# Kernel tuning notes

Measured on AMD Instinct MI355X. Metric: run time of the kernel, lower is better.

Reference implementation:

```python
import jax, jax.numpy as jnp
import numpy as np

B, I, O, D, H = 64, 1152, 32, 8, 16
NUM_ITERS = 3


def squash(s, axis=-1, eps=1e-08):
    sq = jnp.sum(s * s, axis=axis, keepdims=True)
    return (sq / (1.0 + sq)) * s / jnp.sqrt(sq + eps)


def setup_inputs() -> dict:
    key = jax.random.key(0)
    k1, k2 = jax.random.split(key)
    u = jax.random.normal(k1, (B, I, D), dtype=jnp.float32)
    weight = jax.random.normal(k2, (I, O, D, H), dtype=jnp.float32) * 0.1
    return {"u": u, "weight": weight}


def reference(u, weight):
    # u_hat: [b, i, o, h]
    u_hat = jnp.einsum('bid,iodh->bioh', u, weight)
    logits = jnp.zeros(u_hat.shape[:3], dtype=u_hat.dtype)

    def body(logits, _):
        coupling = jax.nn.softmax(logits, axis=-1)        # [b,i,o]
        s = jnp.einsum('bio,bioh->boh', coupling, u_hat)  # [b,o,h]
        v = squash(s)                                     # [b,o,h]
        logits = logits + jnp.einsum('boh,bioh->bio', v, u_hat)
        return logits, v

    _, vs = jax.lax.scan(body, logits, None, length=NUM_ITERS)
    return vs[-1]
```

## Files before the change

### kernel.cpp

```cpp
#include <hip/hip_runtime.h>
#include <hip/hip_bf16.h>

#define BB 64
#define II 1152
#define OO 32
#define DD 8
#define HH 16
#define BOH (BB * OO * HH)
#define WTILE (OO * DD * HH)

#define IC   9
#define NIC  128
#define NBB  16
#define NBG  4
#define NJB  4
#define WS   132

__device__ __forceinline__ float row_sum16(float x)
{
    x += __int_as_float(__builtin_amdgcn_update_dpp(
            0, __float_as_int(x), 0x121, 0xF, 0xF, false));
    x += __int_as_float(__builtin_amdgcn_update_dpp(
            0, __float_as_int(x), 0x122, 0xF, 0xF, false));
    x += __int_as_float(__builtin_amdgcn_update_dpp(
            0, __float_as_int(x), 0x124, 0xF, 0xF, false));
    x += __int_as_float(__builtin_amdgcn_update_dpp(
            0, __float_as_int(x), 0x128, 0xF, 0xF, false));
    return x;
}

__device__ __forceinline__ float o_sum32(float x)
{
    float s = row_sum16(x);
    s += __int_as_float(__builtin_amdgcn_ds_swizzle(__float_as_int(s), 0x401F));
    return s;
}

template<int PASS, bool ATOMIC>
__global__ __launch_bounds__(256)
void pass_kernel(const float* __restrict__ u, const float* __restrict__ w,
                 const float* __restrict__ pv0, const float* __restrict__ pv1,
                 float* __restrict__ out)
{
    __shared__ float Wsh[2][OO * WS];

    const int tid   = threadIdx.x;
    const int o     = tid & 31;
    const int hh    = (tid >> 5) & 1;
    const int bq    = tid >> 6;
    const int bbase = blockIdx.y * NBB;
    const int i0    = blockIdx.x * IC;
    const int hofs  = hh * 8;

    float vsum[NJB][8];
    if (PASS >= 1) {
        #pragma unroll
        for (int jb = 0; jb < NJB; jb++) {
            const int b = bbase + bq * NJB + jb;
            const float* p = pv0 + ((b * OO + o) * HH + hofs);
            float4 a = *(const float4*)p;
            float4 c = *(const float4*)(p + 4);
            vsum[jb][0] = a.x; vsum[jb][1] = a.y; vsum[jb][2] = a.z; vsum[jb][3] = a.w;
            vsum[jb][4] = c.x; vsum[jb][5] = c.y; vsum[jb][6] = c.z; vsum[jb][7] = c.w;
            if (PASS == 2) {
                const float* q = pv1 + ((b * OO + o) * HH + hofs);
                float4 a2 = *(const float4*)q;
                float4 c2 = *(const float4*)(q + 4);
                vsum[jb][0] += a2.x; vsum[jb][1] += a2.y; vsum[jb][2] += a2.z; vsum[jb][3] += a2.w;
                vsum[jb][4] += c2.x; vsum[jb][5] += c2.y; vsum[jb][6] += c2.z; vsum[jb][7] += c2.w;
            }
        }
    }

    float sacc[NJB][8];
    #pragma unroll
    for (int jb = 0; jb < NJB; jb++)
        #pragma unroll
        for (int h2 = 0; h2 < 8; h2++) sacc[jb][h2] = 0.f;

    {
        const float* wg = w + (size_t)i0 * WTILE;
        #pragma unroll
        for (int j = 0; j < 4; j++) {
            const int c = tid + j * 256;
            float4 v4 = *(const float4*)(wg + c * 4);
            *(float4*)&Wsh[0][(c >> 5) * WS + (c & 31) * 4] = v4;
        }
    }
    __syncthreads();

    for (int ii = 0; ii < IC; ii++) {
        const float* wcur = Wsh[ii & 1];
        const bool pf = (ii + 1 < IC);
        float4 t0, t1, t2, t3;
        if (pf) {
            const float* wg = w + (size_t)(i0 + ii + 1) * WTILE;
            t0 = *(const float4*)(wg + (tid      ) * 4);
            t1 = *(const float4*)(wg + (tid + 256) * 4);
            t2 = *(const float4*)(wg + (tid + 512) * 4);
            t3 = *(const float4*)(wg + (tid + 768) * 4);
        }

        float us[NJB][8];
        #pragma unroll
        for (int jb = 0; jb < NJB; jb++) {
            const float* ub = u + ((size_t)(bbase + bq * NJB + jb) * II + (i0 + ii)) * DD;
            float4 a = *(const float4*)ub;
            float4 c = *(const float4*)(ub + 4);
            us[jb][0] = a.x; us[jb][1] = a.y; us[jb][2] = a.z; us[jb][3] = a.w;
            us[jb][4] = c.x; us[jb][5] = c.y; us[jb][6] = c.z; us[jb][7] = c.w;
        }

        float uh[NJB][8];
        #pragma unroll
        for (int jb = 0; jb < NJB; jb++)
            #pragma unroll
            for (int h2 = 0; h2 < 8; h2++) uh[jb][h2] = 0.f;
        #pragma unroll
        for (int d = 0; d < DD; d++) {
            const float* wp = &wcur[o * WS + d * HH + hofs];
            float4 wa = *(const float4*)wp;
            float4 wb = *(const float4*)(wp + 4);
            const float wv[8] = {wa.x, wa.y, wa.z, wa.w, wb.x, wb.y, wb.z, wb.w};
            #pragma unroll
            for (int jb = 0; jb < NJB; jb++)
                #pragma unroll
                for (int h2 = 0; h2 < 8; h2++)
                    uh[jb][h2] = fmaf(us[jb][d], wv[h2], uh[jb][h2]);
        }

        float cc[NJB];
        if (PASS == 0) {
            #pragma unroll
            for (int jb = 0; jb < NJB; jb++) cc[jb] = 1.0f / 32.0f;
        } else {
            #pragma unroll
            for (int jb = 0; jb < NJB; jb++) {
                float lg = 0.f;
                #pragma unroll
                for (int h2 = 0; h2 < 8; h2++)
                    lg = fmaf(vsum[jb][h2], uh[jb][h2], lg);
                lg += __shfl_xor(lg, 32, 64);
                const float e = __expf(lg);
                const float se = o_sum32(e);
                cc[jb] = __fdividef(e, se);
            }
        }

        #pragma unroll
        for (int jb = 0; jb < NJB; jb++)
            #pragma unroll
            for (int h2 = 0; h2 < 8; h2++)
                sacc[jb][h2] = fmaf(cc[jb], uh[jb][h2], sacc[jb][h2]);

        if (pf) {
            float* wn = Wsh[(ii + 1) & 1];
            const int c0 = tid, c1 = tid + 256, c2 = tid + 512, c3 = tid + 768;
            *(float4*)&wn[(c0 >> 5) * WS + (c0 & 31) * 4] = t0;
            *(float4*)&wn[(c1 >> 5) * WS + (c1 & 31) * 4] = t1;
            *(float4*)&wn[(c2 >> 5) * WS + (c2 & 31) * 4] = t2;
            *(float4*)&wn[(c3 >> 5) * WS + (c3 & 31) * 4] = t3;
        }
        __syncthreads();
    }

    #pragma unroll
    for (int jb = 0; jb < NJB; jb++) {
        const int b = bbase + bq * NJB + jb;
        if (ATOMIC) {
            float* p = out + ((b * OO + o) * HH + hofs);
            #pragma unroll
            for (int h2 = 0; h2 < 8; h2++) atomicAdd(p + h2, sacc[jb][h2]);
        } else {
            float* p = out + ((size_t)blockIdx.x * BB + b) * (OO * HH) + o * HH + hofs;
            *(float4*)p       = make_float4(sacc[jb][0], sacc[jb][1], sacc[jb][2], sacc[jb][3]);
            *(float4*)(p + 4) = make_float4(sacc[jb][4], sacc[jb][5], sacc[jb][6], sacc[jb][7]);
        }
    }
}

__global__ __launch_bounds__(256)
void reduce_squash_kernel(const float* __restrict__ part, float* __restrict__ v)
{
    const int t = blockIdx.x * blockDim.x + threadIdx.x;
    float acc = 0.f;
    #pragma unroll 16
    for (int ic = 0; ic < NIC; ic++)
        acc += part[(size_t)ic * BOH + t];
    const float sq = row_sum16(acc * acc);
    const float scale = (sq / (1.f + sq)) * rsqrtf(sq + 1e-8f);
    v[t] = acc * scale;
}

__global__ __launch_bounds__(256)
void squash_kernel(const float* __restrict__ s, float* __restrict__ v)
{
    const int t = blockIdx.x * blockDim.x + threadIdx.x;
    if (t >= BB * OO) return;
    const float4* sp = (const float4*)(s + t * HH);
    float4 a = sp[0], b = sp[1], c = sp[2], d = sp[3];
    float sq = a.x*a.x + a.y*a.y + a.z*a.z + a.w*a.w
             + b.x*b.x + b.y*b.y + b.z*b.z + b.w*b.w
             + c.x*c.x + c.y*c.y + c.z*c.z + c.w*c.w
             + d.x*d.x + d.y*d.y + d.z*d.z + d.w*d.w;
    const float scale = (sq / (1.f + sq)) * rsqrtf(sq + 1e-8f);
    a.x *= scale; a.y *= scale; a.z *= scale; a.w *= scale;
    b.x *= scale; b.y *= scale; b.z *= scale; b.w *= scale;
    c.x *= scale; c.y *= scale; c.z *= scale; c.w *= scale;
    d.x *= scale; d.y *= scale; d.z *= scale; d.w *= scale;
    float4* vp = (float4*)(v + t * HH);
    vp[0] = a; vp[1] = b; vp[2] = c; vp[3] = d;
}

extern "C" void kernel_launch(void* const* d_in, const int* in_sizes, int n_in,
                              void* d_out, int out_size, void* d_ws, size_t ws_size,
                              hipStream_t stream)
{
    (void)in_sizes; (void)n_in; (void)out_size;
    const float* u = (const float*)d_in[0];
    const float* w = (const float*)d_in[1];
    float* out = (float*)d_out;

    const size_t need = ((size_t)NIC * BOH + 2 * BOH) * sizeof(float);
    const dim3 grid(NIC, NBG), blk(256);

    if (ws_size >= need) {
        float* part = (float*)d_ws;
        float* v0   = part + (size_t)NIC * BOH;
        float* v1   = v0 + BOH;
        const int rblocks = BOH / 256;

        pass_kernel<0, false><<<grid, blk, 0, stream>>>(u, w, nullptr, nullptr, part);
        reduce_squash_kernel<<<rblocks, 256, 0, stream>>>(part, v0);
        pass_kernel<1, false><<<grid, blk, 0, stream>>>(u, w, v0, nullptr, part);
        reduce_squash_kernel<<<rblocks, 256, 0, stream>>>(part, v1);
        pass_kernel<2, false><<<grid, blk, 0, stream>>>(u, w, v0, v1, part);
        reduce_squash_kernel<<<rblocks, 256, 0, stream>>>(part, out);
    } else {
        float* s0 = (float*)d_ws;
        float* s1 = s0 + BOH;
        float* v0 = s1 + BOH;
        float* v1 = v0 + BOH;
        hipMemsetAsync(d_ws, 0, 2 * BOH * sizeof(float), stream);
        hipMemsetAsync(d_out, 0, BOH * sizeof(float), stream);
        const int sq_blocks = (BB * OO + 255) / 256;

        pass_kernel<0, true><<<grid, blk, 0, stream>>>(u, w, nullptr, nullptr, s0);
        squash_kernel<<<sq_blocks, 256, 0, stream>>>(s0, v0);
        pass_kernel<1, true><<<grid, blk, 0, stream>>>(u, w, v0, nullptr, s1);
        squash_kernel<<<sq_blocks, 256, 0, stream>>>(s1, v1);
        pass_kernel<2, true><<<grid, blk, 0, stream>>>(u, w, v0, v1, out);
        squash_kernel<<<sq_blocks, 256, 0, stream>>>(out, out);
    }
}
```

Measured before the change: 142.1 us.

## Convert weights to bf16 in first pass and reuse for later routing passes

The first pass now also writes a bf16 copy of the weight tensor to workspace. Passes 1 and 2 run a new kernel that reads the half-size bf16 weights, converts them to fp32 in registers, and splits the input dimension into more chunks (192 instead of 128) for more parallelism. The goal is to halve weight memory traffic in the later passes, at the cost of reduced weight precision, extra writes in pass 0, a larger workspace, and a larger partial-sum reduction.

Measured after the change: 186.8 us. 31.4% more time.

```diff
diff --git a/kernel.cpp b/kernel.cpp
--- a/kernel.cpp
+++ b/kernel.cpp
@@ -9,26 +9,34 @@
 #define BOH (BB * OO * HH)
 #define WTILE (OO * DD * HH)
 
-#define IC   9
-#define NIC  128
+#define IC0  9
+#define NIC0 128
+#define IC2  6
+#define NIC2 192
 #define NBB  16
 #define NBG  4
 #define NJB  4
 #define WS   132
+#define WSB  136
+#define TBF  4352
+
+__device__ __forceinline__ unsigned bfpack(float a, float b)
+{
+    unsigned ua = __float_as_uint(a); ua += 0x7FFFu + ((ua >> 16) & 1u);
+    unsigned ub = __float_as_uint(b); ub += 0x7FFFu + ((ub >> 16) & 1u);
+    return (ua >> 16) | (ub & 0xFFFF0000u);
+}
+__device__ __forceinline__ float bflo(unsigned x) { return __uint_as_float(x << 16); }
+__device__ __forceinline__ float bfhi(unsigned x) { return __uint_as_float(x & 0xFFFF0000u); }
 
 __device__ __forceinline__ float row_sum16(float x)
 {
-    x += __int_as_float(__builtin_amdgcn_update_dpp(
-            0, __float_as_int(x), 0x121, 0xF, 0xF, false));
-    x += __int_as_float(__builtin_amdgcn_update_dpp(
-            0, __float_as_int(x), 0x122, 0xF, 0xF, false));
-    x += __int_as_float(__builtin_amdgcn_update_dpp(
-            0, __float_as_int(x), 0x124, 0xF, 0xF, false));
-    x += __int_as_float(__builtin_amdgcn_update_dpp(
-            0, __float_as_int(x), 0x128, 0xF, 0xF, false));
+    x += __int_as_float(__builtin_amdgcn_update_dpp(0, __float_as_int(x), 0x121, 0xF, 0xF, false));
+    x += __int_as_float(__builtin_amdgcn_update_dpp(0, __float_as_int(x), 0x122, 0xF, 0xF, false));
+    x += __int_as_float(__builtin_amdgcn_update_dpp(0, __float_as_int(x), 0x124, 0xF, 0xF, false));
+    x += __int_as_float(__builtin_amdgcn_update_dpp(0, __float_as_int(x), 0x128, 0xF, 0xF, false));
     return x;
 }
-
 __device__ __forceinline__ float o_sum32(float x)
 {
     float s = row_sum16(x);
@@ -40,7 +48,7 @@
 __global__ __launch_bounds__(256)
 void pass_kernel(const float* __restrict__ u, const float* __restrict__ w,
                  const float* __restrict__ pv0, const float* __restrict__ pv1,
-                 float* __restrict__ out)
+                 float* __restrict__ out, unsigned* __restrict__ wb)
 {
     __shared__ float Wsh[2][OO * WS];
 
@@ -49,8 +57,9 @@
     const int hh    = (tid >> 5) & 1;
     const int bq    = tid >> 6;
     const int bbase = blockIdx.y * NBB;
-    const int i0    = blockIdx.x * IC;
+    const int i0    = blockIdx.x * IC0;
     const int hofs  = hh * 8;
+    const bool cvt  = (wb != nullptr) && (blockIdx.y == 0);
 
     float vsum[NJB][8];
     if (PASS >= 1) {
@@ -85,13 +94,17 @@
             const int c = tid + j * 256;
             float4 v4 = *(const float4*)(wg + c * 4);
             *(float4*)&Wsh[0][(c >> 5) * WS + (c & 31) * 4] = v4;
+            if (cvt) {
+                uint2 p2 = make_uint2(bfpack(v4.x, v4.y), bfpack(v4.z, v4.w));
+                *(uint2*)(wb + (size_t)i0 * 2048 + c * 2) = p2;
+            }
         }
     }
     __syncthreads();
 
-    for (int ii = 0; ii < IC; ii++) {
+    for (int ii = 0; ii < IC0; ii++) {
         const float* wcur = Wsh[ii & 1];
-        const bool pf = (ii + 1 < IC);
+        const bool pf = (ii + 1 < IC0);
         float4 t0, t1, t2, t3;
         if (pf) {
             const float* wg = w + (size_t)(i0 + ii + 1) * WTILE;
@@ -120,8 +133,8 @@
         for (int d = 0; d < DD; d++) {
             const float* wp = &wcur[o * WS + d * HH + hofs];
             float4 wa = *(const float4*)wp;
-            float4 wb = *(const float4*)(wp + 4);
-            const float wv[8] = {wa.x, wa.y, wa.z, wa.w, wb.x, wb.y, wb.z, wb.w};
+            float4 wc = *(const float4*)(wp + 4);
+            const float wv[8] = {wa.x, wa.y, wa.z, wa.w, wc.x, wc.y, wc.z, wc.w};
             #pragma unroll
             for (int jb = 0; jb < NJB; jb++)
                 #pragma unroll
@@ -160,6 +173,13 @@
             *(float4*)&wn[(c1 >> 5) * WS + (c1 & 31) * 4] = t1;
             *(float4*)&wn[(c2 >> 5) * WS + (c2 & 31) * 4] = t2;
             *(float4*)&wn[(c3 >> 5) * WS + (c3 & 31) * 4] = t3;
+            if (cvt) {
+                unsigned* wt = wb + (size_t)(i0 + ii + 1) * 2048;
+                *(uint2*)(wt + c0 * 2) = make_uint2(bfpack(t0.x, t0.y), bfpack(t0.z, t0.w));
+                *(uint2*)(wt + c1 * 2) = make_uint2(bfpack(t1.x, t1.y), bfpack(t1.z, t1.w));
+                *(uint2*)(wt + c2 * 2) = make_uint2(bfpack(t2.x, t2.y), bfpack(t2.z, t2.w));
+                *(uint2*)(wt + c3 * 2) = make_uint2(bfpack(t3.x, t3.y), bfpack(t3.z, t3.w));
+            }
         }
         __syncthreads();
     }
@@ -179,13 +199,152 @@
     }
 }
 
+template<int PASS>
+__global__ __launch_bounds__(256)
+void pass_bf(const float* __restrict__ u, const unsigned* __restrict__ wb,
+             const float* __restrict__ pv0, const float* __restrict__ pv1,
+             float* __restrict__ out)
+{
+    __shared__ unsigned short Wb[2][2 * TBF];
+
+    const int tid   = threadIdx.x;
+    const int o     = tid & 31;
+    const int hh    = (tid >> 5) & 1;
+    const int bq    = tid >> 6;
+    const int bbase = blockIdx.y * NBB;
+    const int i0    = blockIdx.x * IC2;
+    const int hofs  = hh * 8;
+
+    float vsum[NJB][8];
+    #pragma unroll
+    for (int jb = 0; jb < NJB; jb++) {
+        const int b = bbase + bq * NJB + jb;
+        const float* p = pv0 + ((b * OO + o) * HH + hofs);
+        float4 a = *(const float4*)p;
+        float4 c = *(const float4*)(p + 4);
+        vsum[jb][0] = a.x; vsum[jb][1] = a.y; vsum[jb][2] = a.z; vsum[jb][3] = a.w;
+        vsum[jb][4] = c.x; vsum[jb][5] = c.y; vsum[jb][6] = c.z; vsum[jb][7] = c.w;
+        if (PASS == 2) {
+            const float* q = pv1 + ((b * OO + o) * HH + hofs);
+            float4 a2 = *(const float4*)q;
+            float4 c2 = *(const float4*)(q + 4);
+            vsum[jb][0] += a2.x; vsum[jb][1] += a2.y; vsum[jb][2] += a2.z; vsum[jb][3] += a2.w;
+            vsum[jb][4] += c2.x; vsum[jb][5] += c2.y; vsum[jb][6] += c2.z; vsum[jb][7] += c2.w;
+        }
+    }
+
+    float sacc[NJB][8];
+    #pragma unroll
+    for (int jb = 0; jb < NJB; jb++)
+        #pragma unroll
+        for (int h2 = 0; h2 < 8; h2++) sacc[jb][h2] = 0.f;
+
+    {
+        const uint4* wg = (const uint4*)(wb + (size_t)i0 * 2048);
+        #pragma unroll
+        for (int j = 0; j < 4; j++) {
+            const int c  = tid + j * 256;
+            uint4 v4 = wg[c];
+            const int cc = c & 511;
+            *(uint4*)&Wb[0][(c >> 9) * TBF + (cc >> 4) * WSB + (cc & 15) * 8] = v4;
+        }
+    }
+    __syncthreads();
+
+    for (int s = 0; s < IC2 / 2; s++) {
+        const unsigned short* wbuf = Wb[s & 1];
+        const bool pf = (s + 1 < IC2 / 2);
+        uint4 t0, t1, t2, t3;
+        if (pf) {
+            const uint4* wg = (const uint4*)(wb + (size_t)(i0 + 2 * s + 2) * 2048);
+            t0 = wg[tid];
+            t1 = wg[tid + 256];
+            t2 = wg[tid + 512];
+            t3 = wg[tid + 768];
+        }
+
+        #pragma unroll
+        for (int it = 0; it < 2; it++) {
+            const int i = i0 + 2 * s + it;
+            const unsigned short* wt = &wbuf[it * TBF + o * WSB + hofs];
+
+            float us[NJB][8];
+            #pragma unroll
+            for (int jb = 0; jb < NJB; jb++) {
+                const float* ub = u + ((size_t)(bbase + bq * NJB + jb) * II + i) * DD;
+                float4 a = *(const float4*)ub;
+                float4 c = *(const float4*)(ub + 4);
+                us[jb][0] = a.x; us[jb][1] = a.y; us[jb][2] = a.z; us[jb][3] = a.w;
+                us[jb][4] = c.x; us[jb][5] = c.y; us[jb][6] = c.z; us[jb][7] = c.w;
+            }
+
+            float uh[NJB][8];
+            #pragma unroll
+            for (int jb = 0; jb < NJB; jb++)
+                #pragma unroll
+                for (int h2 = 0; h2 < 8; h2++) uh[jb][h2] = 0.f;
+            #pragma unroll
+            for (int d = 0; d < DD; d++) {
+                const uint4 wd = *(const uint4*)&wt[d * HH];
+                const float wv[8] = { bflo(wd.x), bfhi(wd.x), bflo(wd.y), bfhi(wd.y),
+                                      bflo(wd.z), bfhi(wd.z), bflo(wd.w), bfhi(wd.w) };
+                #pragma unroll
+                for (int jb = 0; jb < NJB; jb++)
+                    #pragma unroll
+                    for (int h2 = 0; h2 < 8; h2++)
+                        uh[jb][h2] = fmaf(us[jb][d], wv[h2], uh[jb][h2]);
+            }
+
+            float cc[NJB];
+            #pragma unroll
+            for (int jb = 0; jb < NJB; jb++) {
+                float lg = 0.f;
+                #pragma unroll
+                for (int h2 = 0; h2 < 8; h2++)
+                    lg = fmaf(vsum[jb][h2], uh[jb][h2], lg);
+                lg += __shfl_xor(lg, 32, 64);
+                const float e = __expf(lg);
+                const float se = o_sum32(e);
+                cc[jb] = __fdividef(e, se);
+            }
+
+            #pragma unroll
+            for (int jb = 0; jb < NJB; jb++)
+                #pragma unroll
+                for (int h2 = 0; h2 < 8; h2++)
+                    sacc[jb][h2] = fmaf(cc[jb], uh[jb][h2], sacc[jb][h2]);
+        }
+
+        if (pf) {
+            unsigned short* wn = Wb[(s + 1) & 1];
+            #pragma unroll
+            for (int j = 0; j < 4; j++) {
+                const int c  = tid + j * 256;
+                const int cc = c & 511;
+                uint4 v4 = (j == 0) ? t0 : (j == 1) ? t1 : (j == 2) ? t2 : t3;
+                *(uint4*)&wn[(c >> 9) * TBF + (cc >> 4) * WSB + (cc & 15) * 8] = v4;
+            }
+            __syncthreads();
+        }
+    }
+
+    #pragma unroll
+    for (int jb = 0; jb < NJB; jb++) {
+        const int b = bbase + bq * NJB + jb;
+        float* p = out + ((size_t)blockIdx.x * BB + b) * (OO * HH) + o * HH + hofs;
+        *(float4*)p       = make_float4(sacc[jb][0], sacc[jb][1], sacc[jb][2], sacc[jb][3]);
+        *(float4*)(p + 4) = make_float4(sacc[jb][4], sacc[jb][5], sacc[jb][6], sacc[jb][7]);
+    }
+}
+
+template<int NCH>
 __global__ __launch_bounds__(256)
 void reduce_squash_kernel(const float* __restrict__ part, float* __restrict__ v)
 {
     const int t = blockIdx.x * blockDim.x + threadIdx.x;
     float acc = 0.f;
     #pragma unroll 16
-    for (int ic = 0; ic < NIC; ic++)
+    for (int ic = 0; ic < NCH; ic++)
         acc += part[(size_t)ic * BOH + t];
     const float sq = row_sum16(acc * acc);
     const float scale = (sq / (1.f + sq)) * rsqrtf(sq + 1e-8f);
@@ -221,21 +380,22 @@
     const float* w = (const float*)d_in[1];
     float* out = (float*)d_out;
 
-    const size_t need = ((size_t)NIC * BOH + 2 * BOH) * sizeof(float);
-    const dim3 grid(NIC, NBG), blk(256);
+    const size_t wb_dwords = (size_t)II * 2048;
+    const size_t need = wb_dwords * 4 + ((size_t)NIC2 * BOH + 2 * BOH) * 4;
 
     if (ws_size >= need) {
-        float* part = (float*)d_ws;
-        float* v0   = part + (size_t)NIC * BOH;
+        unsigned* wbp = (unsigned*)d_ws;
+        float* part = (float*)d_ws + wb_dwords;
+        float* v0   = part + (size_t)NIC2 * BOH;
         float* v1   = v0 + BOH;
         const int rblocks = BOH / 256;
 
-        pass_kernel<0, false><<<grid, blk, 0, stream>>>(u, w, nullptr, nullptr, part);
-        reduce_squash_kernel<<<rblocks, 256, 0, stream>>>(part, v0);
-        pass_kernel<1, false><<<grid, blk, 0, stream>>>(u, w, v0, nullptr, part);
-        reduce_squash_kernel<<<rblocks, 256, 0, stream>>>(part, v1);
-        pass_kernel<2, false><<<grid, blk, 0, stream>>>(u, w, v0, v1, part);
-        reduce_squash_kernel<<<rblocks, 256, 0, stream>>>(part, out);
+        pass_kernel<0, false><<<dim3(NIC0, NBG), 256, 0, stream>>>(u, w, nullptr, nullptr, part, wbp);
+        reduce_squash_kernel<NIC0><<<rblocks, 256, 0, stream>>>(part, v0);
+        pass_bf<1><<<dim3(NIC2, NBG), 256, 0, stream>>>(u, wbp, v0, nullptr, part);
+        reduce_squash_kernel<NIC2><<<rblocks, 256, 0, stream>>>(part, v1);
+        pass_bf<2><<<dim3(NIC2, NBG), 256, 0, stream>>>(u, wbp, v0, v1, part);
+        reduce_squash_kernel<NIC2><<<rblocks, 256, 0, stream>>>(part, out);
     } else {
         float* s0 = (float*)d_ws;
         float* s1 = s0 + BOH;
@@ -245,11 +405,11 @@
         hipMemsetAsync(d_out, 0, BOH * sizeof(float), stream);
         const int sq_blocks = (BB * OO + 255) / 256;
 
-        pass_kernel<0, true><<<grid, blk, 0, stream>>>(u, w, nullptr, nullptr, s0);
+        pass_kernel<0, true><<<dim3(NIC0, NBG), 256, 0, stream>>>(u, w, nullptr, nullptr, s0, nullptr);
         squash_kernel<<<sq_blocks, 256, 0, stream>>>(s0, v0);
-        pass_kernel<1, true><<<grid, blk, 0, stream>>>(u, w, v0, nullptr, s1);
+        pass_kernel<1, true><<<dim3(NIC0, NBG), 256, 0, stream>>>(u, w, v0, nullptr, s1, nullptr);
         squash_kernel<<<sq_blocks, 256, 0, stream>>>(s1, v1);
-        pass_kernel<2, true><<<grid, blk, 0, stream>>>(u, w, v0, v1, out);
+        pass_kernel<2, true><<<dim3(NIC0, NBG), 256, 0, stream>>>(u, w, v0, v1, out, nullptr);
         squash_kernel<<<sq_blocks, 256, 0, stream>>>(out, out);
     }
 }
```
